# Kernel tuning notes

Hardware: AMD Instinct MI355X
Metric: run time of the kernel (lower is better)

Reference implementation:

```python
import jax, jax.numpy as jnp
import numpy as np

B, H, S, D = 2, 12, 4096, 768
BS = 64              # block size
HD = D // H          # head dim = 64
NB = S // BS         # 64 blocks
MC = 3               # max graph connections per block
PEN = -10000.0
RSQRT_D = 1.0 / np.sqrt(HD).astype(np.float32)


def setup_inputs() -> dict:
    key = jax.random.key(0)
    ks = jax.random.split(key, 6)
    hidden_states = jax.random.normal(ks[0], (B, S, D), jnp.float32)
    Wq = jax.random.normal(ks[1], (D, D), jnp.float32) * 0.02
    Wk = jax.random.normal(ks[2], (D, D), jnp.float32) * 0.02
    Wv = jax.random.normal(ks[3], (D, D), jnp.float32) * 0.02
    Wo = jax.random.normal(ks[4], (D, D), jnp.float32) * 0.02
    graph_attn = jax.random.randint(ks[5], (B, H, NB, MC), 0, NB, jnp.int32)
    return dict(
        hidden_states=hidden_states, Wq=Wq, Wk=Wk, Wv=Wv, Wo=Wo,
        band_mask=jnp.ones((B, 1, NB - 4, BS, 3 * BS), jnp.float32),
        from_mask=jnp.ones((B, 1, S, 1), jnp.float32),
        to_mask=jnp.ones((B, 1, 1, S), jnp.float32),
        from_blocked_mask=jnp.ones((B, NB, BS), jnp.float32),
        to_blocked_mask=jnp.ones((B, NB, BS), jnp.float32),
        graph_attn=graph_attn,
    )


def reference(hidden_states, Wq, Wk, Wv, Wo, band_mask, from_mask, to_mask,
              from_blocked_mask, to_blocked_mask, graph_attn):
    def proj(W):  # [B,S,D] -> [B,H,S,HD]
        return (hidden_states @ W.T).reshape(B, S, H, HD).transpose(0, 2, 1, 3)

    q, k, v = proj(Wq), proj(Wk), proj(Wv)
    bq = q.reshape(B, H, NB, BS, HD)
    bk = k.reshape(B, H, NB, BS, HD)
    bv = v.reshape(B, H, NB, BS, HD)

    # gather graph-selected key/value blocks: [B,H,NB,MC*BS,HD]
    gather = jax.vmap(jax.vmap(lambda blocks, idx: blocks[idx]))
    gk = gather(bk, graph_attn).reshape(B, H, NB, MC * BS, HD)
    gv = gather(bv, graph_attn).reshape(B, H, NB, MC * BS, HD)

    # graph mask from blocked masks: [B,H,NB,BS,MC*BS]
    gm = jax.vmap(lambda tm, ga: tm[ga])(to_blocked_mask, graph_attn)  # [B,H,NB,MC,BS]
    gm = gm.reshape(B, H, NB, MC * BS)
    graph_mask = jnp.einsum('blq,bhlk->bhlqk', from_blocked_mask, gm)

    # ---- first block: global attention over all keys ----
    fp = jnp.einsum('bhqd,bhkd->bhqk', bq[:, :, 0], k) * RSQRT_D + (1.0 - to_mask) * PEN
    first_ctx = jnp.einsum('bhqk,bhkd->bhqd', jax.nn.softmax(fp, -1), v)[:, :, None]

    # ---- second block: blocks 0,1,2,last + graph-gathered ----
    sk = jnp.concatenate([bk[:, :, 0], bk[:, :, 1], bk[:, :, 2], bk[:, :, -1], gk[:, :, 1]], axis=2)
    sv = jnp.concatenate([bv[:, :, 0], bv[:, :, 1], bv[:, :, 2], bv[:, :, -1], gv[:, :, 1]], axis=2)
    sp = jnp.einsum('bhqd,bhkd->bhqk', bq[:, :, 1], sk) * RSQRT_D
    seq_pad = jnp.concatenate([to_mask[:, :, :, :3 * BS], to_mask[:, :, :, -BS:],
                               jnp.ones((B, 1, 1, MC * BS), to_mask.dtype)], axis=3)
    rand_pad = jnp.concatenate([jnp.ones((B, H, BS, 4 * BS), graph_mask.dtype),
                                graph_mask[:, :, 1]], axis=3)
    sp = sp + (1.0 - jnp.minimum(seq_pad, rand_pad)) * PEN
    second_ctx = jnp.einsum('bhqk,bhkd->bhqd', jax.nn.softmax(sp, -1), sv)[:, :, None]

    # ---- middle blocks: sliding window (3 blocks) + first + last + graph ----
    ek = jnp.concatenate([bk[:, :, 1:-3], bk[:, :, 2:-2], bk[:, :, 3:-1]], axis=3)  # [B,H,NB-4,3BS,HD]
    ev = jnp.concatenate([bv[:, :, 1:-3], bv[:, :, 2:-2], bv[:, :, 3:-1]], axis=3)
    qm = bq[:, :, 2:-2]
    inner = jnp.einsum('bhlqd,bhlkd->bhlqk', qm, ek) * RSQRT_D + (1.0 - band_mask) * PEN
    randp = jnp.einsum('bhlqd,bhlkd->bhlqk', qm, gk[:, :, 2:-2]) * RSQRT_D + (1.0 - graph_mask[:, :, 2:-2]) * PEN
    firstp = jnp.einsum('bhlqd,bhkd->bhlqk', qm, bk[:, :, 0]) * RSQRT_D + (1.0 - to_mask[:, :, :, None, :BS]) * PEN
    lastp = jnp.einsum('bhlqd,bhkd->bhlqk', qm, bk[:, :, -1]) * RSQRT_D + (1.0 - to_mask[:, :, :, None, -BS:]) * PEN
    band = jnp.concatenate([firstp, inner, randp, lastp], axis=-1)
    attn = jax.nn.softmax(band, -1)
    mid_ctx = (jnp.einsum('bhlqk,bhlkd->bhlqd', attn[..., BS:4 * BS], ev)
               + jnp.einsum('bhlqk,bhlkd->bhlqd', attn[..., 4 * BS:4 * BS + MC * BS], gv[:, :, 2:-2])
               + jnp.einsum('bhlqk,bhkd->bhlqd', attn[..., :BS], bv[:, :, 0])
               + jnp.einsum('bhlqk,bhkd->bhlqd', attn[..., -BS:], bv[:, :, -1]))

    # ---- second-to-last block ----
    slk = jnp.concatenate([bk[:, :, 0], bk[:, :, -3], bk[:, :, -2], bk[:, :, -1], gk[:, :, -2]], axis=2)
    slv = jnp.concatenate([bv[:, :, 0], bv[:, :, -3], bv[:, :, -2], bv[:, :, -1], gv[:, :, -2]], axis=2)
    slp = jnp.einsum('bhqd,bhkd->bhqk', bq[:, :, -2], slk) * RSQRT_D
    sl_seq = jnp.concatenate([to_mask[:, :, :, :BS], to_mask[:, :, :, -3 * BS:],
                              jnp.ones((B, 1, 1, MC * BS), to_mask.dtype)], axis=3)
    sl_rand = jnp.concatenate([jnp.ones((B, H, BS, 4 * BS), graph_mask.dtype),
                               graph_mask[:, :, -2]], axis=3)
    slp = slp + (1.0 - jnp.minimum(sl_seq, sl_rand)) * PEN
    sl_ctx = jnp.einsum('bhqk,bhkd->bhqd', jax.nn.softmax(slp, -1), slv)[:, :, None]

    # ---- last block: global attention over all keys ----
    lp = jnp.einsum('bhqd,bhkd->bhqk', bq[:, :, -1], k) * RSQRT_D + (1.0 - to_mask) * PEN
    last_ctx = jnp.einsum('bhqk,bhkd->bhqd', jax.nn.softmax(lp, -1), v)[:, :, None]

    ctx = jnp.concatenate([first_ctx, second_ctx, mid_ctx, sl_ctx, last_ctx], axis=2)
    ctx = ctx.reshape(B, H, S, HD) * from_mask            # [B,H,S,HD]
    ctx = ctx.transpose(0, 2, 1, 3).reshape(B, S, D)      # [B,S,D]
    return ctx @ Wo.T                                     # output projection (no bias)
```

## Files before the change

kernel.cpp:

```cpp
#include <hip/hip_runtime.h>
#include <hip/hip_bf16.h>

#define BB 2
#define HH 12
#define SS 4096
#define DD 768
#define HD 64
#define NBK 64
#define MC 3

typedef __attribute__((ext_vector_type(8))) short short8_t;
typedef __attribute__((ext_vector_type(4))) float float4_t;

__device__ __forceinline__ unsigned short f2bf(float f) {
  union { float f; unsigned u; } c;
  c.f = f;
  unsigned u = c.u + 0x7FFFu + ((c.u >> 16) & 1u);
  return (unsigned short)(u >> 16);
}

__device__ __forceinline__ void gload16(const unsigned short* gp,
                                        unsigned short* lp) {
  __builtin_amdgcn_global_load_lds(
      (const __attribute__((address_space(1))) unsigned int*)gp,
      (__attribute__((address_space(3))) unsigned int*)lp, 16, 0, 0);
}

#define LDK 72

__global__ __launch_bounds__(256) void cvt_all(
    const float* __restrict__ hs, const float* __restrict__ Wq,
    const float* __restrict__ Wk, const float* __restrict__ Wv,
    const float* __restrict__ Wo, unsigned short* __restrict__ hsb,
    unsigned short* __restrict__ wqkvb, unsigned short* __restrict__ wob) {
  long i4 = (long)blockIdx.x * 256 + threadIdx.x;
  const float* src;
  unsigned short* dst;
  if (i4 < 1572864) {
    src = hs + i4 * 4;
    dst = hsb + i4 * 4;
  } else {
    long r = i4 - 1572864;
    int w = (int)(r / 147456);
    long e = r % 147456;
    src = (w == 0 ? Wq : w == 1 ? Wk : w == 2 ? Wv : Wo) + e * 4;
    dst = (w < 3) ? (wqkvb + (long)w * 589824 + e * 4) : (wob + e * 4);
  }
  float4_t v = *(const float4_t*)src;
  uint2 p;
  p.x = (unsigned)f2bf(v[0]) | ((unsigned)f2bf(v[1]) << 16);
  p.y = (unsigned)f2bf(v[2]) | ((unsigned)f2bf(v[3]) << 16);
  *(uint2*)dst = p;
}

#define STAGE_T(buf_, A_, B_, m0_, n0_, kt_)                                  \
  {                                                                           \
    int rr_ = lane >> 3;                                                      \
    int cg_ = (lane & 7) ^ rr_;                                               \
    _Pragma("unroll") for (int u = 0; u < 4; u++) {                           \
      int g_ = w * 4 + u;                                                     \
      gload16(A_ + (size_t)(m0_ + g_ * 8 + rr_) * DD + kt_ + cg_ * 8,         \
              &As[buf_][g_ * 512]);                                           \
    }                                                                         \
    _Pragma("unroll") for (int u = 0; u < 2; u++) {                           \
      int g_ = w * 2 + u;                                                     \
      gload16(B_ + (size_t)(n0_ + g_ * 8 + rr_) * DD + kt_ + cg_ * 8,         \
              &Bs[buf_][g_ * 512]);                                           \
    }                                                                         \
  }

#define LOAD_FRAGS2(buf_, kk_)                                                \
  int cb = qd + ((kk_) >> 3);                                                 \
  short8_t af[2], bfr[4];                                                     \
  _Pragma("unroll") for (int i = 0; i < 2; i++) {                             \
    int r_ = wm + i * 16 + fr;                                                \
    af[i] = *(const short8_t*)&As[buf_][r_ * 64 + (cb ^ (fr & 7)) * 8];       \
  }                                                                           \
  _Pragma("unroll") for (int j = 0; j < 4; j++) {                             \
    int r_ = j * 16 + fr;                                                     \
    bfr[j] = *(const short8_t*)&Bs[buf_][r_ * 64 + (cb ^ (fr & 7)) * 8];      \
  }

__global__ __launch_bounds__(256) void gemm_qkv_b(
    const unsigned short* __restrict__ A, const unsigned short* __restrict__ W,
    unsigned short* __restrict__ qb, unsigned short* __restrict__ kb,
    unsigned short* __restrict__ vtb) {
  __shared__ unsigned short As[2][128 * 64];
  __shared__ unsigned short Bs[2][64 * 64];
  int tid = threadIdx.x;
  int m0 = blockIdx.x * 128;
  int n0 = blockIdx.y * 64;
  int lane = tid & 63;
  int w = tid >> 6;
  int wm = w * 32;
  int fr = lane & 15;
  int qd = lane >> 4;
  int ysel = n0 / 768;

  float4_t acc[8];
#pragma unroll
  for (int i = 0; i < 8; i++)
#pragma unroll
    for (int r = 0; r < 4; r++) acc[i][r] = 0.f;

  STAGE_T(0, A, W, m0, n0, 0)
  int p = 0;

  if (ysel < 2) {
    for (int kt = 0; kt < DD; kt += 64) {
      __syncthreads();
      if (kt + 64 < DD) STAGE_T(p ^ 1, A, W, m0, n0, kt + 64)
#pragma unroll
      for (int kk = 0; kk < 64; kk += 32) {
        LOAD_FRAGS2(p, kk)
#pragma unroll
        for (int i = 0; i < 2; i++)
#pragma unroll
          for (int j = 0; j < 4; j++)
            acc[j * 2 + i] = __builtin_amdgcn_mfma_f32_16x16x32_bf16(
                bfr[j], af[i], acc[j * 2 + i], 0, 0, 0);
      }
      p ^= 1;
    }
    int cn = lane & 15;
    int quad = lane >> 4;
    float scale = (ysel == 0) ? 0.125f : 1.0f;
    unsigned short* dst = (ysel == 0) ? qb : kb;
    int nb0 = n0 - ysel * 768;
#pragma unroll
    for (int j = 0; j < 4; j++)
#pragma unroll
      for (int i = 0; i < 2; i++) {
        int m = m0 + wm + i * 16 + cn;
        int nn = nb0 + j * 16 + quad * 4;
        int b = m >> 12, s = m & 4095;
        int h = nn >> 6, d0 = nn & 63;
        uint2 pk;
        pk.x = (unsigned)f2bf(acc[j * 2 + i][0] * scale) |
               ((unsigned)f2bf(acc[j * 2 + i][1] * scale) << 16);
        pk.y = (unsigned)f2bf(acc[j * 2 + i][2] * scale) |
               ((unsigned)f2bf(acc[j * 2 + i][3] * scale) << 16);
        *(uint2*)&dst[(((size_t)b * HH + h) * SS + s) * HD + d0] = pk;
      }
  } else {
    for (int kt = 0; kt < DD; kt += 64) {
      __syncthreads();
      if (kt + 64 < DD) STAGE_T(p ^ 1, A, W, m0, n0, kt + 64)
#pragma unroll
      for (int kk = 0; kk < 64; kk += 32) {
        LOAD_FRAGS2(p, kk)
#pragma unroll
        for (int i = 0; i < 2; i++)
#pragma unroll
          for (int j = 0; j < 4; j++)
            acc[i * 4 + j] = __builtin_amdgcn_mfma_f32_16x16x32_bf16(
                af[i], bfr[j], acc[i * 4 + j], 0, 0, 0);
      }
      p ^= 1;
    }
    int cn = lane & 15;
    int quad = lane >> 4;
    int nb0 = n0 - 1536;
#pragma unroll
    for (int i = 0; i < 2; i++)
#pragma unroll
      for (int j = 0; j < 4; j++) {
        int m = m0 + wm + i * 16 + quad * 4;
        int nn = nb0 + j * 16 + cn;
        int b = m >> 12, s0 = m & 4095;
        int h = nn >> 6, d = nn & 63;
        uint2 pk;
        pk.x = (unsigned)f2bf(acc[i * 4 + j][0]) |
               ((unsigned)f2bf(acc[i * 4 + j][1]) << 16);
        pk.y = (unsigned)f2bf(acc[i * 4 + j][2]) |
               ((unsigned)f2bf(acc[i * 4 + j][3]) << 16);
        *(uint2*)&vtb[(((size_t)b * HH + h) * HD + d) * SS + s0] = pk;
      }
  }
}

__global__ __launch_bounds__(256) void gemm_out_b(
    const unsigned short* __restrict__ A, const unsigned short* __restrict__ W,
    float* __restrict__ dst) {
  __shared__ unsigned short As[2][128 * 64];
  __shared__ unsigned short Bs[2][64 * 64];
  int tid = threadIdx.x;
  int m0 = blockIdx.x * 128;
  int n0 = blockIdx.y * 64;
  int lane = tid & 63;
  int w = tid >> 6;
  int wm = w * 32;
  int fr = lane & 15;
  int qd = lane >> 4;

  float4_t acc[8];
#pragma unroll
  for (int i = 0; i < 8; i++)
#pragma unroll
    for (int r = 0; r < 4; r++) acc[i][r] = 0.f;

  STAGE_T(0, A, W, m0, n0, 0)
  int p = 0;
  for (int kt = 0; kt < DD; kt += 64) {
    __syncthreads();
    if (kt + 64 < DD) STAGE_T(p ^ 1, A, W, m0, n0, kt + 64)
#pragma unroll
    for (int kk = 0; kk < 64; kk += 32) {
      LOAD_FRAGS2(p, kk)
#pragma unroll
      for (int i = 0; i < 2; i++)
#pragma unroll
        for (int j = 0; j < 4; j++)
          acc[i * 4 + j] = __builtin_amdgcn_mfma_f32_16x16x32_bf16(
              af[i], bfr[j], acc[i * 4 + j], 0, 0, 0);
    }
    p ^= 1;
  }

  int cn = lane & 15;
  int rb = (lane >> 4) * 4;
#pragma unroll
  for (int i = 0; i < 2; i++)
#pragma unroll
    for (int j = 0; j < 4; j++)
#pragma unroll
      for (int r = 0; r < 4; r++) {
        int m = m0 + wm + i * 16 + rb + r;
        int n = n0 + j * 16 + cn;
        dst[(size_t)m * DD + n] = acc[i * 4 + j][r];
      }
}

__global__ __launch_bounds__(256) void attn2(
    const unsigned short* __restrict__ q, const unsigned short* __restrict__ k,
    const unsigned short* __restrict__ vt, const int* __restrict__ graph,
    unsigned short* __restrict__ ctxb, float* __restrict__ part) {
  __shared__ unsigned short Ks[2][64 * LDK];
  __shared__ unsigned short Vs[2][64 * LDK];
  __shared__ unsigned short Ps[4][16 * LDK];

  int tid = threadIdx.x;
  int id = blockIdx.x;
  int b, h, l, nkb, heavy, chunk = 0, hid = 0;
  int list[8];
  if (id < 384) {
    heavy = 1;
    hid = id >> 3;
    chunk = id & 7;
    b = hid / 24;
    int r = hid % 24;
    h = r >> 1;
    l = (r & 1) ? (NBK - 1) : 0;
    nkb = 8;
#pragma unroll
    for (int i = 0; i < 8; i++) list[i] = chunk * 8 + i;
  } else {
    heavy = 0;
    int j = id - 384;
    b = j / 744;
    int r = j % 744;
    h = r / 62;
    l = 1 + r % 62;
    const int* g = graph + (((size_t)b * HH + h) * NBK + l) * MC;
    int n = 0;
    if (l == 1) {
      list[0] = 0; list[1] = 1; list[2] = 2; list[3] = NBK - 1; n = 4;
    } else if (l == NBK - 2) {
      list[0] = 0; list[1] = NBK - 3; list[2] = NBK - 2; list[3] = NBK - 1; n = 4;
    } else {
      list[0] = 0; list[1] = l - 1; list[2] = l; list[3] = l + 1;
      list[4] = NBK - 1; n = 5;
    }
    for (int m = 0; m < MC; m++) list[n++] = g[m];
    nkb = n;
  }
  size_t base = ((size_t)b * HH + h) * SS * HD;

  int lane = tid & 63;
  int w = tid >> 6;
  int lr = lane & 15;
  int quad = lane >> 4;

  short8_t qa[2];
  {
    const unsigned short* qp =
        q + base + (size_t)(l * 64 + w * 16 + lr) * HD + quad * 8;
    qa[0] = *(const short8_t*)qp;
    qa[1] = *(const short8_t*)(qp + 32);
  }

  float4_t Ot[4];
  float ls[4];
#pragma unroll
  for (int t = 0; t < 4; t++)
#pragma unroll
    for (int r = 0; r < 4; r++) Ot[t][r] = 0.f;
#pragma unroll
  for (int r = 0; r < 4; r++) ls[r] = 0.f;

  int srow = tid >> 3;
  int scol = (tid & 7) * 8;

  uint4 kr0, kr1, vr0, vr1;
  {
    int kb = list[0];
    const unsigned short* kp = k + base + (size_t)(kb * 64 + srow) * HD + scol;
    const unsigned short* vp = vt + base + (size_t)srow * SS + kb * 64 + scol;
    kr0 = *(const uint4*)kp;
    kr1 = *(const uint4*)(kp + 32 * HD);
    vr0 = *(const uint4*)vp;
    vr1 = *(const uint4*)(vp + 32 * SS);
  }
  *(uint4*)&Ks[0][srow * LDK + scol] = kr0;
  *(uint4*)&Ks[0][(srow + 32) * LDK + scol] = kr1;
  *(uint4*)&Vs[0][srow * LDK + scol] = vr0;
  *(uint4*)&Vs[0][(srow + 32) * LDK + scol] = vr1;
  int p = 0;

  for (int t = 0; t < nkb; t++) {
    __syncthreads();

    if (t + 1 < nkb) {
      int kb = list[t + 1];
      const unsigned short* kp = k + base + (size_t)(kb * 64 + srow) * HD + scol;
      const unsigned short* vp = vt + base + (size_t)srow * SS + kb * 64 + scol;
      kr0 = *(const uint4*)kp;
      kr1 = *(const uint4*)(kp + 32 * HD);
      vr0 = *(const uint4*)vp;
      vr1 = *(const uint4*)(vp + 32 * SS);
    }

    float4_t st[4];
#pragma unroll
    for (int tt = 0; tt < 4; tt++) {
#pragma unroll
      for (int r = 0; r < 4; r++) st[tt][r] = 0.f;
      short8_t kb0 = *(const short8_t*)&Ks[p][(tt * 16 + lr) * LDK + quad * 8];
      short8_t kb1 =
          *(const short8_t*)&Ks[p][(tt * 16 + lr) * LDK + quad * 8 + 32];
      st[tt] = __builtin_amdgcn_mfma_f32_16x16x32_bf16(qa[0], kb0, st[tt], 0, 0, 0);
      st[tt] = __builtin_amdgcn_mfma_f32_16x16x32_bf16(qa[1], kb1, st[tt], 0, 0, 0);
    }

#pragma unroll
    for (int tt = 0; tt < 4; tt++)
#pragma unroll
      for (int r = 0; r < 4; r++) {
        float pv = __expf(st[tt][r]);
        st[tt][r] = pv;
        ls[r] += pv;
        Ps[w][(quad * 4 + r) * LDK + tt * 16 + lr] = f2bf(pv);
      }

#pragma unroll
    for (int s = 0; s < 2; s++) {
      short8_t pa = *(const short8_t*)&Ps[w][lr * LDK + s * 32 + quad * 8];
#pragma unroll
      for (int tt = 0; tt < 4; tt++) {
        short8_t vb =
            *(const short8_t*)&Vs[p][(tt * 16 + lr) * LDK + s * 32 + quad * 8];
        Ot[tt] = __builtin_amdgcn_mfma_f32_16x16x32_bf16(pa, vb, Ot[tt], 0, 0, 0);
      }
    }

    if (t + 1 < nkb) {
      *(uint4*)&Ks[p ^ 1][srow * LDK + scol] = kr0;
      *(uint4*)&Ks[p ^ 1][(srow + 32) * LDK + scol] = kr1;
      *(uint4*)&Vs[p ^ 1][srow * LDK + scol] = vr0;
      *(uint4*)&Vs[p ^ 1][(srow + 32) * LDK + scol] = vr1;
    }
    p ^= 1;
  }

#pragma unroll
  for (int r = 0; r < 4; r++)
#pragma unroll
    for (int off = 1; off < 16; off <<= 1) ls[r] += __shfl_xor(ls[r], off);

  if (!heavy) {
#pragma unroll
    for (int r = 0; r < 4; r++) {
      float inv = 1.f / ls[r];
      size_t row = (size_t)b * SS + (size_t)l * 64 + w * 16 + quad * 4 + r;
#pragma unroll
      for (int tt = 0; tt < 4; tt++)
        ctxb[row * DD + h * HD + tt * 16 + lr] = f2bf(Ot[tt][r] * inv);
    }
  } else {
    float* pb = part + ((size_t)hid * 8 + chunk) * 4160;
#pragma unroll
    for (int r = 0; r < 4; r++) {
      int rowi = w * 16 + quad * 4 + r;
#pragma unroll
      for (int tt = 0; tt < 4; tt++)
        pb[rowi * 64 + tt * 16 + lr] = Ot[tt][r];
      if (lr == 0) pb[4096 + rowi] = ls[r];
    }
  }
}

__global__ __launch_bounds__(256) void reduce_heavy(
    const float* __restrict__ part, unsigned short* __restrict__ ctxb) {
  __shared__ float lrow[64];
  int hid = blockIdx.x;
  int tid = threadIdx.x;
  int b = hid / 24;
  int r = hid % 24;
  int h = r >> 1;
  int l = (r & 1) ? (NBK - 1) : 0;
  const float* pb = part + (size_t)hid * 8 * 4160;
  if (tid < 64) {
    float s = 0.f;
#pragma unroll
    for (int c = 0; c < 8; c++) s += pb[c * 4160 + 4096 + tid];
    lrow[tid] = s;
  }
  __syncthreads();
#pragma unroll
  for (int e = tid; e < 4096; e += 256) {
    float o = 0.f;
#pragma unroll
    for (int c = 0; c < 8; c++) o += pb[c * 4160 + e];
    int rowi = e >> 6, col = e & 63;
    size_t row = (size_t)b * SS + (size_t)l * 64 + rowi;
    ctxb[row * DD + h * HD + col] = f2bf(o / lrow[rowi]);
  }
}

extern "C" void kernel_launch(void* const* d_in, const int* in_sizes, int n_in,
                              void* d_out, int out_size, void* d_ws,
                              size_t ws_size, hipStream_t stream) {
  const float* hs = (const float*)d_in[0];
  const float* Wq = (const float*)d_in[1];
  const float* Wk = (const float*)d_in[2];
  const float* Wv = (const float*)d_in[3];
  const float* Wo = (const float*)d_in[4];
  const int* graph = (const int*)d_in[10];

  const size_t NHS = (size_t)BB * SS * DD;
  unsigned short* hsb = (unsigned short*)d_ws;
  unsigned short* wqkvb = hsb + NHS;
  unsigned short* wob = wqkvb + 3 * 768 * 768;
  unsigned short* qb = wob + 768 * 768;
  unsigned short* kb = qb + NHS;
  unsigned short* vtb = kb + NHS;
  unsigned short* ctxb = vtb + NHS;
  float* part = (float*)(ctxb + NHS);

  cvt_all<<<8448, 256, 0, stream>>>(hs, Wq, Wk, Wv, Wo, hsb, wqkvb, wob);
  gemm_qkv_b<<<dim3(64, 36, 1), 256, 0, stream>>>(hsb, wqkvb, qb, kb, vtb);
  attn2<<<1872, 256, 0, stream>>>(qb, kb, vtb, graph, ctxb, part);
  reduce_heavy<<<48, 256, 0, stream>>>(part, ctxb);
  gemm_out_b<<<dim3(64, 12, 1), 256, 0, stream>>>(ctxb, wob, (float*)d_out);
}
```

Baseline: 209.5 us.

## Fuse all stages into one persistent cooperative kernel with grid syncs

Replaces the five separate launches (convert, QKV GEMM, attention, heavy-row reduce, output GEMM) with a single persistent cooperative kernel. Blocks loop over virtual tiles per stage and use grid.sync between stages. The goal is to remove kernel launch gaps and inter-kernel drain. In exchange, the grid is capped by occupancy, the grid-wide barriers add cost, and the unified 48KB shared buffer may lower occupancy for the attention stage. The old multi-kernel path is kept as a fallback if the cooperative launch fails.

```diff
diff --git a/kernel.cpp b/kernel.cpp
--- a/kernel.cpp
+++ b/kernel.cpp
@@ -1,5 +1,8 @@
 #include <hip/hip_runtime.h>
 #include <hip/hip_bf16.h>
+#include <hip/hip_cooperative_groups.h>
+
+namespace cg = cooperative_groups;
 
 #define BB 2
 #define HH 12
@@ -8,6 +11,7 @@
 #define HD 64
 #define NBK 64
 #define MC 3
+#define LDK 72
 
 typedef __attribute__((ext_vector_type(8))) short short8_t;
 typedef __attribute__((ext_vector_type(4))) float float4_t;
@@ -26,7 +30,433 @@
       (__attribute__((address_space(3))) unsigned int*)lp, 16, 0, 0);
 }
 
-#define LDK 72
+
+__device__ __forceinline__ void stage_ab(unsigned short* AsB, unsigned short* BsB,
+                                         const unsigned short* A,
+                                         const unsigned short* B, int m0,
+                                         int n0, int kt, int lane, int w) {
+  int rr = lane >> 3;
+  int cgx = (lane & 7) ^ rr;
+#pragma unroll
+  for (int u = 0; u < 4; u++) {
+    int g = w * 4 + u;
+    gload16(A + (size_t)(m0 + g * 8 + rr) * DD + kt + cgx * 8, AsB + g * 512);
+  }
+#pragma unroll
+  for (int u = 0; u < 2; u++) {
+    int g = w * 2 + u;
+    gload16(B + (size_t)(n0 + g * 8 + rr) * DD + kt + cgx * 8, BsB + g * 512);
+  }
+}
+
+template <int SWAP>
+__device__ __forceinline__ void gemm_core(const unsigned short* A,
+                                          const unsigned short* B, int m0,
+                                          int n0, unsigned short* smem,
+                                          int tid, float4_t acc[8]) {
+  unsigned short* As = smem;
+  unsigned short* Bs = smem + 16384;
+  int lane = tid & 63;
+  int w = tid >> 6;
+  int wm = w * 32;
+  int fr = lane & 15;
+  int qd = lane >> 4;
+#pragma unroll
+  for (int i = 0; i < 8; i++)
+#pragma unroll
+    for (int r = 0; r < 4; r++) acc[i][r] = 0.f;
+  __syncthreads();
+  stage_ab(As, Bs, A, B, m0, n0, 0, lane, w);
+  int p = 0;
+  for (int kt = 0; kt < DD; kt += 64) {
+    __syncthreads();
+    if (kt + 64 < DD)
+      stage_ab(As + (p ^ 1) * 8192, Bs + (p ^ 1) * 4096, A, B, m0, n0, kt + 64,
+               lane, w);
+#pragma unroll
+    for (int kk = 0; kk < 64; kk += 32) {
+      int cb = qd + (kk >> 3);
+      short8_t af[2], bfr[4];
+#pragma unroll
+      for (int i = 0; i < 2; i++) {
+        int r_ = wm + i * 16 + fr;
+        af[i] =
+            *(const short8_t*)&As[p * 8192 + r_ * 64 + (cb ^ (fr & 7)) * 8];
+      }
+#pragma unroll
+      for (int j = 0; j < 4; j++) {
+        int r_ = j * 16 + fr;
+        bfr[j] =
+            *(const short8_t*)&Bs[p * 4096 + r_ * 64 + (cb ^ (fr & 7)) * 8];
+      }
+#pragma unroll
+      for (int i = 0; i < 2; i++)
+#pragma unroll
+        for (int j = 0; j < 4; j++) {
+          if (SWAP)
+            acc[j * 2 + i] = __builtin_amdgcn_mfma_f32_16x16x32_bf16(
+                bfr[j], af[i], acc[j * 2 + i], 0, 0, 0);
+          else
+            acc[i * 4 + j] = __builtin_amdgcn_mfma_f32_16x16x32_bf16(
+                af[i], bfr[j], acc[i * 4 + j], 0, 0, 0);
+        }
+    }
+    p ^= 1;
+  }
+}
+
+__device__ __forceinline__ void qkv_tile(int vb, const unsigned short* hsb,
+                                         const unsigned short* wqkvb,
+                                         unsigned short* qb,
+                                         unsigned short* kb,
+                                         unsigned short* vtb,
+                                         unsigned short* smem, int tid) {
+  int m0 = (vb & 63) * 128;
+  int n0 = (vb >> 6) * 64;
+  int ysel = n0 / 768;
+  int lane = tid & 63;
+  int w = tid >> 6;
+  int wm = w * 32;
+  float4_t acc[8];
+  if (ysel < 2) {
+    gemm_core<1>(hsb, wqkvb, m0, n0, smem, tid, acc);
+    int cn = lane & 15;
+    int quad = lane >> 4;
+    float scale = (ysel == 0) ? 0.125f : 1.0f;
+    unsigned short* dst = (ysel == 0) ? qb : kb;
+    int nb0 = n0 - ysel * 768;
+#pragma unroll
+    for (int j = 0; j < 4; j++)
+#pragma unroll
+      for (int i = 0; i < 2; i++) {
+        int m = m0 + wm + i * 16 + cn;
+        int nn = nb0 + j * 16 + quad * 4;
+        int b = m >> 12, s = m & 4095;
+        int h = nn >> 6, d0 = nn & 63;
+        uint2 pk;
+        pk.x = (unsigned)f2bf(acc[j * 2 + i][0] * scale) |
+               ((unsigned)f2bf(acc[j * 2 + i][1] * scale) << 16);
+        pk.y = (unsigned)f2bf(acc[j * 2 + i][2] * scale) |
+               ((unsigned)f2bf(acc[j * 2 + i][3] * scale) << 16);
+        *(uint2*)&dst[(((size_t)b * HH + h) * SS + s) * HD + d0] = pk;
+      }
+  } else {
+    gemm_core<0>(hsb, wqkvb, m0, n0, smem, tid, acc);
+    int cn = lane & 15;
+    int quad = lane >> 4;
+    int nb0 = n0 - 1536;
+#pragma unroll
+    for (int i = 0; i < 2; i++)
+#pragma unroll
+      for (int j = 0; j < 4; j++) {
+        int m = m0 + wm + i * 16 + quad * 4;
+        int nn = nb0 + j * 16 + cn;
+        int b = m >> 12, s0 = m & 4095;
+        int h = nn >> 6, d = nn & 63;
+        uint2 pk;
+        pk.x = (unsigned)f2bf(acc[i * 4 + j][0]) |
+               ((unsigned)f2bf(acc[i * 4 + j][1]) << 16);
+        pk.y = (unsigned)f2bf(acc[i * 4 + j][2]) |
+               ((unsigned)f2bf(acc[i * 4 + j][3]) << 16);
+        *(uint2*)&vtb[(((size_t)b * HH + h) * HD + d) * SS + s0] = pk;
+      }
+  }
+}
+
+__device__ __forceinline__ void out_tile(int vb, const unsigned short* ctxb,
+                                         const unsigned short* wob,
+                                         float* dst, unsigned short* smem,
+                                         int tid) {
+  int m0 = (vb & 63) * 128;
+  int n0 = (vb >> 6) * 64;
+  float4_t acc[8];
+  gemm_core<0>(ctxb, wob, m0, n0, smem, tid, acc);
+  int lane = tid & 63;
+  int w = tid >> 6;
+  int wm = w * 32;
+  int cn = lane & 15;
+  int rb = (lane >> 4) * 4;
+#pragma unroll
+  for (int i = 0; i < 2; i++)
+#pragma unroll
+    for (int j = 0; j < 4; j++)
+#pragma unroll
+      for (int r = 0; r < 4; r++) {
+        int m = m0 + wm + i * 16 + rb + r;
+        int n = n0 + j * 16 + cn;
+        dst[(size_t)m * DD + n] = acc[i * 4 + j][r];
+      }
+}
+
+__device__ __forceinline__ void attn_one(int id, const unsigned short* q,
+                                         const unsigned short* k,
+                                         const unsigned short* vt,
+                                         const int* graph,
+                                         unsigned short* ctxb, float* part,
+                                         unsigned short* smem, int tid) {
+  unsigned short* Ks = smem;
+  unsigned short* Vs = smem + 2 * 64 * LDK;
+  unsigned short* Ps = smem + 4 * 64 * LDK;
+  int b, h, l, nkb, heavy, chunk = 0, hid = 0;
+  int list[8];
+  if (id < 384) {
+    heavy = 1;
+    hid = id >> 3;
+    chunk = id & 7;
+    b = hid / 24;
+    int r = hid % 24;
+    h = r >> 1;
+    l = (r & 1) ? (NBK - 1) : 0;
+    nkb = 8;
+#pragma unroll
+    for (int i = 0; i < 8; i++) list[i] = chunk * 8 + i;
+  } else {
+    heavy = 0;
+    int j = id - 384;
+    b = j / 744;
+    int r = j % 744;
+    h = r / 62;
+    l = 1 + r % 62;
+    const int* g = graph + (((size_t)b * HH + h) * NBK + l) * MC;
+    int n = 0;
+    if (l == 1) {
+      list[0] = 0; list[1] = 1; list[2] = 2; list[3] = NBK - 1; n = 4;
+    } else if (l == NBK - 2) {
+      list[0] = 0; list[1] = NBK - 3; list[2] = NBK - 2; list[3] = NBK - 1;
+      n = 4;
+    } else {
+      list[0] = 0; list[1] = l - 1; list[2] = l; list[3] = l + 1;
+      list[4] = NBK - 1; n = 5;
+    }
+    for (int m = 0; m < MC; m++) list[n++] = g[m];
+    nkb = n;
+  }
+  size_t base = ((size_t)b * HH + h) * SS * HD;
+
+  int lane = tid & 63;
+  int w = tid >> 6;
+  int lr = lane & 15;
+  int quad = lane >> 4;
+
+  short8_t qa[2];
+  {
+    const unsigned short* qp =
+        q + base + (size_t)(l * 64 + w * 16 + lr) * HD + quad * 8;
+    qa[0] = *(const short8_t*)qp;
+    qa[1] = *(const short8_t*)(qp + 32);
+  }
+
+  float4_t Ot[4];
+  float ls[4];
+#pragma unroll
+  for (int t = 0; t < 4; t++)
+#pragma unroll
+    for (int r = 0; r < 4; r++) Ot[t][r] = 0.f;
+#pragma unroll
+  for (int r = 0; r < 4; r++) ls[r] = 0.f;
+
+  int srow = tid >> 3;
+  int scol = (tid & 7) * 8;
+
+  uint4 kr0, kr1, vr0, vr1;
+  {
+    int kb = list[0];
+    const unsigned short* kp = k + base + (size_t)(kb * 64 + srow) * HD + scol;
+    const unsigned short* vp = vt + base + (size_t)srow * SS + kb * 64 + scol;
+    kr0 = *(const uint4*)kp;
+    kr1 = *(const uint4*)(kp + 32 * HD);
+    vr0 = *(const uint4*)vp;
+    vr1 = *(const uint4*)(vp + 32 * SS);
+  }
+  __syncthreads();
+  *(uint4*)&Ks[srow * LDK + scol] = kr0;
+  *(uint4*)&Ks[(srow + 32) * LDK + scol] = kr1;
+  *(uint4*)&Vs[srow * LDK + scol] = vr0;
+  *(uint4*)&Vs[(srow + 32) * LDK + scol] = vr1;
+  int p = 0;
+
+  for (int t = 0; t < nkb; t++) {
+    __syncthreads();
+
+    if (t + 1 < nkb) {
+      int kb = list[t + 1];
+      const unsigned short* kp =
+          k + base + (size_t)(kb * 64 + srow) * HD + scol;
+      const unsigned short* vp =
+          vt + base + (size_t)srow * SS + kb * 64 + scol;
+      kr0 = *(const uint4*)kp;
+      kr1 = *(const uint4*)(kp + 32 * HD);
+      vr0 = *(const uint4*)vp;
+      vr1 = *(const uint4*)(vp + 32 * SS);
+    }
+
+    float4_t st[4];
+#pragma unroll
+    for (int tt = 0; tt < 4; tt++) {
+#pragma unroll
+      for (int r = 0; r < 4; r++) st[tt][r] = 0.f;
+      short8_t kb0 =
+          *(const short8_t*)&Ks[p * 4608 + (tt * 16 + lr) * LDK + quad * 8];
+      short8_t kb1 = *(const short8_t*)&Ks[p * 4608 + (tt * 16 + lr) * LDK +
+                                           quad * 8 + 32];
+      st[tt] =
+          __builtin_amdgcn_mfma_f32_16x16x32_bf16(qa[0], kb0, st[tt], 0, 0, 0);
+      st[tt] =
+          __builtin_amdgcn_mfma_f32_16x16x32_bf16(qa[1], kb1, st[tt], 0, 0, 0);
+    }
+
+#pragma unroll
+    for (int tt = 0; tt < 4; tt++)
+#pragma unroll
+      for (int r = 0; r < 4; r++) {
+        float pv = __expf(st[tt][r]);
+        st[tt][r] = pv;
+        ls[r] += pv;
+        Ps[w * 1152 + (quad * 4 + r) * LDK + tt * 16 + lr] = f2bf(pv);
+      }
+
+#pragma unroll
+    for (int s = 0; s < 2; s++) {
+      short8_t pa =
+          *(const short8_t*)&Ps[w * 1152 + lr * LDK + s * 32 + quad * 8];
+#pragma unroll
+      for (int tt = 0; tt < 4; tt++) {
+        short8_t vb = *(const short8_t*)&Vs[p * 4608 + (tt * 16 + lr) * LDK +
+                                            s * 32 + quad * 8];
+        Ot[tt] =
+            __builtin_amdgcn_mfma_f32_16x16x32_bf16(pa, vb, Ot[tt], 0, 0, 0);
+      }
+    }
+
+    if (t + 1 < nkb) {
+      int pn = p ^ 1;
+      *(uint4*)&Ks[pn * 4608 + srow * LDK + scol] = kr0;
+      *(uint4*)&Ks[pn * 4608 + (srow + 32) * LDK + scol] = kr1;
+      *(uint4*)&Vs[pn * 4608 + srow * LDK + scol] = vr0;
+      *(uint4*)&Vs[pn * 4608 + (srow + 32) * LDK + scol] = vr1;
+    }
+    p ^= 1;
+  }
+
+#pragma unroll
+  for (int r = 0; r < 4; r++)
+#pragma unroll
+    for (int off = 1; off < 16; off <<= 1) ls[r] += __shfl_xor(ls[r], off);
+
+  if (!heavy) {
+#pragma unroll
+    for (int r = 0; r < 4; r++) {
+      float inv = 1.f / ls[r];
+      size_t row = (size_t)b * SS + (size_t)l * 64 + w * 16 + quad * 4 + r;
+#pragma unroll
+      for (int tt = 0; tt < 4; tt++)
+        ctxb[row * DD + h * HD + tt * 16 + lr] = f2bf(Ot[tt][r] * inv);
+    }
+  } else {
+    float* pb = part + ((size_t)hid * 8 + chunk) * 4160;
+#pragma unroll
+    for (int r = 0; r < 4; r++) {
+      int rowi = w * 16 + quad * 4 + r;
+#pragma unroll
+      for (int tt = 0; tt < 4; tt++)
+        pb[rowi * 64 + tt * 16 + lr] = Ot[tt][r];
+      if (lr == 0) pb[4096 + rowi] = ls[r];
+    }
+  }
+}
+
+__device__ __forceinline__ void reduce_one(int hid, const float* part,
+                                           unsigned short* ctxb,
+                                           unsigned short* smem, int tid) {
+  float* lrow = (float*)smem;
+  int b = hid / 24;
+  int r = hid % 24;
+  int h = r >> 1;
+  int l = (r & 1) ? (NBK - 1) : 0;
+  const float* pb = part + (size_t)hid * 8 * 4160;
+  __syncthreads();
+  if (tid < 64) {
+    float s = 0.f;
+#pragma unroll
+    for (int c = 0; c < 8; c++) s += pb[c * 4160 + 4096 + tid];
+    lrow[tid] = s;
+  }
+  __syncthreads();
+  for (int e = tid; e < 4096; e += 256) {
+    float o = 0.f;
+#pragma unroll
+    for (int c = 0; c < 8; c++) o += pb[c * 4160 + e];
+    int rowi = e >> 6, col = e & 63;
+    size_t row = (size_t)b * SS + (size_t)l * 64 + rowi;
+    ctxb[row * DD + h * HD + col] = f2bf(o / lrow[rowi]);
+  }
+  __syncthreads();
+}
+
+__global__ __launch_bounds__(256) void fused_all(
+    const float* __restrict__ hs, const float* __restrict__ Wq,
+    const float* __restrict__ Wk, const float* __restrict__ Wv,
+    const float* __restrict__ Wo, const int* __restrict__ graph,
+    float* __restrict__ dst, unsigned short* __restrict__ wsu) {
+  __shared__ __align__(16) unsigned short smem[24576];
+  int tid = threadIdx.x;
+  int wg = blockIdx.x;
+  int gsz = gridDim.x;
+  const size_t NHS = (size_t)BB * SS * DD;
+  unsigned short* hsb = wsu;
+  unsigned short* wqkvb = hsb + NHS;
+  unsigned short* wob = wqkvb + 3 * 768 * 768;
+  unsigned short* qb = wob + 768 * 768;
+  unsigned short* kb = qb + NHS;
+  unsigned short* vtb = kb + NHS;
+  unsigned short* ctxb = vtb + NHS;
+  float* part = (float*)(ctxb + NHS);
+  cg::grid_group grid = cg::this_grid();
+
+  for (long i4 = (long)wg * 256 + tid; i4 < 2162688; i4 += (long)gsz * 256) {
+    const float* src;
+    unsigned short* dp;
+    if (i4 < 1572864) {
+      src = hs + i4 * 4;
+      dp = hsb + i4 * 4;
+    } else {
+      long r = i4 - 1572864;
+      int wsel = (int)(r / 147456);
+      long e = r % 147456;
+      src = (wsel == 0 ? Wq : wsel == 1 ? Wk : wsel == 2 ? Wv : Wo) + e * 4;
+      dp = (wsel < 3) ? (wqkvb + (long)wsel * 589824 + e * 4) : (wob + e * 4);
+    }
+    float4_t v = *(const float4_t*)src;
+    uint2 pk;
+    pk.x = (unsigned)f2bf(v[0]) | ((unsigned)f2bf(v[1]) << 16);
+    pk.y = (unsigned)f2bf(v[2]) | ((unsigned)f2bf(v[3]) << 16);
+    *(uint2*)dp = pk;
+  }
+  __threadfence();
+  grid.sync();
+  __threadfence();
+
+  for (int vb = wg; vb < 2304; vb += gsz)
+    qkv_tile(vb, hsb, wqkvb, qb, kb, vtb, smem, tid);
+  __threadfence();
+  grid.sync();
+  __threadfence();
+
+  for (int vb = wg; vb < 1872; vb += gsz)
+    attn_one(vb, qb, kb, vtb, graph, ctxb, part, smem, tid);
+  __threadfence();
+  grid.sync();
+  __threadfence();
+
+  for (int vb = wg; vb < 48; vb += gsz) reduce_one(vb, part, ctxb, smem, tid);
+  __threadfence();
+  grid.sync();
+  __threadfence();
+
+  for (int vb = wg; vb < 768; vb += gsz)
+    out_tile(vb, ctxb, wob, dst, smem, tid);
+}
+
 
 __global__ __launch_bounds__(256) void cvt_all(
     const float* __restrict__ hs, const float* __restrict__ Wq,
@@ -53,378 +483,35 @@
   *(uint2*)dst = p;
 }
 
-#define STAGE_T(buf_, A_, B_, m0_, n0_, kt_)                                  \
-  {                                                                           \
-    int rr_ = lane >> 3;                                                      \
-    int cg_ = (lane & 7) ^ rr_;                                               \
-    _Pragma("unroll") for (int u = 0; u < 4; u++) {                           \
-      int g_ = w * 4 + u;                                                     \
-      gload16(A_ + (size_t)(m0_ + g_ * 8 + rr_) * DD + kt_ + cg_ * 8,         \
-              &As[buf_][g_ * 512]);                                           \
-    }                                                                         \
-    _Pragma("unroll") for (int u = 0; u < 2; u++) {                           \
-      int g_ = w * 2 + u;                                                     \
-      gload16(B_ + (size_t)(n0_ + g_ * 8 + rr_) * DD + kt_ + cg_ * 8,         \
-              &Bs[buf_][g_ * 512]);                                           \
-    }                                                                         \
-  }
-
-#define LOAD_FRAGS2(buf_, kk_)                                                \
-  int cb = qd + ((kk_) >> 3);                                                 \
-  short8_t af[2], bfr[4];                                                     \
-  _Pragma("unroll") for (int i = 0; i < 2; i++) {                             \
-    int r_ = wm + i * 16 + fr;                                                \
-    af[i] = *(const short8_t*)&As[buf_][r_ * 64 + (cb ^ (fr & 7)) * 8];       \
-  }                                                                           \
-  _Pragma("unroll") for (int j = 0; j < 4; j++) {                             \
-    int r_ = j * 16 + fr;                                                     \
-    bfr[j] = *(const short8_t*)&Bs[buf_][r_ * 64 + (cb ^ (fr & 7)) * 8];      \
-  }
-
 __global__ __launch_bounds__(256) void gemm_qkv_b(
     const unsigned short* __restrict__ A, const unsigned short* __restrict__ W,
     unsigned short* __restrict__ qb, unsigned short* __restrict__ kb,
     unsigned short* __restrict__ vtb) {
-  __shared__ unsigned short As[2][128 * 64];
-  __shared__ unsigned short Bs[2][64 * 64];
-  int tid = threadIdx.x;
-  int m0 = blockIdx.x * 128;
-  int n0 = blockIdx.y * 64;
-  int lane = tid & 63;
-  int w = tid >> 6;
-  int wm = w * 32;
-  int fr = lane & 15;
-  int qd = lane >> 4;
-  int ysel = n0 / 768;
-
-  float4_t acc[8];
-#pragma unroll
-  for (int i = 0; i < 8; i++)
-#pragma unroll
-    for (int r = 0; r < 4; r++) acc[i][r] = 0.f;
-
-  STAGE_T(0, A, W, m0, n0, 0)
-  int p = 0;
-
-  if (ysel < 2) {
-    for (int kt = 0; kt < DD; kt += 64) {
-      __syncthreads();
-      if (kt + 64 < DD) STAGE_T(p ^ 1, A, W, m0, n0, kt + 64)
-#pragma unroll
-      for (int kk = 0; kk < 64; kk += 32) {
-        LOAD_FRAGS2(p, kk)
-#pragma unroll
-        for (int i = 0; i < 2; i++)
-#pragma unroll
-          for (int j = 0; j < 4; j++)
-            acc[j * 2 + i] = __builtin_amdgcn_mfma_f32_16x16x32_bf16(
-                bfr[j], af[i], acc[j * 2 + i], 0, 0, 0);
-      }
-      p ^= 1;
-    }
-    int cn = lane & 15;
-    int quad = lane >> 4;
-    float scale = (ysel == 0) ? 0.125f : 1.0f;
-    unsigned short* dst = (ysel == 0) ? qb : kb;
-    int nb0 = n0 - ysel * 768;
-#pragma unroll
-    for (int j = 0; j < 4; j++)
-#pragma unroll
-      for (int i = 0; i < 2; i++) {
-        int m = m0 + wm + i * 16 + cn;
-        int nn = nb0 + j * 16 + quad * 4;
-        int b = m >> 12, s = m & 4095;
-        int h = nn >> 6, d0 = nn & 63;
-        uint2 pk;
-        pk.x = (unsigned)f2bf(acc[j * 2 + i][0] * scale) |
-               ((unsigned)f2bf(acc[j * 2 + i][1] * scale) << 16);
-        pk.y = (unsigned)f2bf(acc[j * 2 + i][2] * scale) |
-               ((unsigned)f2bf(acc[j * 2 + i][3] * scale) << 16);
-        *(uint2*)&dst[(((size_t)b * HH + h) * SS + s) * HD + d0] = pk;
-      }
-  } else {
-    for (int kt = 0; kt < DD; kt += 64) {
-      __syncthreads();
-      if (kt + 64 < DD) STAGE_T(p ^ 1, A, W, m0, n0, kt + 64)
-#pragma unroll
-      for (int kk = 0; kk < 64; kk += 32) {
-        LOAD_FRAGS2(p, kk)
-#pragma unroll
-        for (int i = 0; i < 2; i++)
-#pragma unroll
-          for (int j = 0; j < 4; j++)
-            acc[i * 4 + j] = __builtin_amdgcn_mfma_f32_16x16x32_bf16(
-                af[i], bfr[j], acc[i * 4 + j], 0, 0, 0);
-      }
-      p ^= 1;
-    }
-    int cn = lane & 15;
-    int quad = lane >> 4;
-    int nb0 = n0 - 1536;
-#pragma unroll
-    for (int i = 0; i < 2; i++)
-#pragma unroll
-      for (int j = 0; j < 4; j++) {
-        int m = m0 + wm + i * 16 + quad * 4;
-        int nn = nb0 + j * 16 + cn;
-        int b = m >> 12, s0 = m & 4095;
-        int h = nn >> 6, d = nn & 63;
-        uint2 pk;
-        pk.x = (unsigned)f2bf(acc[i * 4 + j][0]) |
-               ((unsigned)f2bf(acc[i * 4 + j][1]) << 16);
-        pk.y = (unsigned)f2bf(acc[i * 4 + j][2]) |
-               ((unsigned)f2bf(acc[i * 4 + j][3]) << 16);
-        *(uint2*)&vtb[(((size_t)b * HH + h) * HD + d) * SS + s0] = pk;
-      }
-  }
+  __shared__ __align__(16) unsigned short smem[24576];
+  int vb = blockIdx.x + blockIdx.y * 64;
+  qkv_tile(vb, A, W, qb, kb, vtb, smem, threadIdx.x);
 }
 
 __global__ __launch_bounds__(256) void gemm_out_b(
     const unsigned short* __restrict__ A, const unsigned short* __restrict__ W,
     float* __restrict__ dst) {
-  __shared__ unsigned short As[2][128 * 64];
-  __shared__ unsigned short Bs[2][64 * 64];
-  int tid = threadIdx.x;
-  int m0 = blockIdx.x * 128;
-  int n0 = blockIdx.y * 64;
-  int lane = tid & 63;
-  int w = tid >> 6;
-  int wm = w * 32;
-  int fr = lane & 15;
-  int qd = lane >> 4;
-
-  float4_t acc[8];
-#pragma unroll
-  for (int i = 0; i < 8; i++)
-#pragma unroll
-    for (int r = 0; r < 4; r++) acc[i][r] = 0.f;
-
-  STAGE_T(0, A, W, m0, n0, 0)
-  int p = 0;
-  for (int kt = 0; kt < DD; kt += 64) {
-    __syncthreads();
-    if (kt + 64 < DD) STAGE_T(p ^ 1, A, W, m0, n0, kt + 64)
-#pragma unroll
-    for (int kk = 0; kk < 64; kk += 32) {
-      LOAD_FRAGS2(p, kk)
-#pragma unroll
-      for (int i = 0; i < 2; i++)
-#pragma unroll
-        for (int j = 0; j < 4; j++)
-          acc[i * 4 + j] = __builtin_amdgcn_mfma_f32_16x16x32_bf16(
-              af[i], bfr[j], acc[i * 4 + j], 0, 0, 0);
-    }
-    p ^= 1;
-  }
-
-  int cn = lane & 15;
-  int rb = (lane >> 4) * 4;
-#pragma unroll
-  for (int i = 0; i < 2; i++)
-#pragma unroll
-    for (int j = 0; j < 4; j++)
-#pragma unroll
-      for (int r = 0; r < 4; r++) {
-        int m = m0 + wm + i * 16 + rb + r;
-        int n = n0 + j * 16 + cn;
-        dst[(size_t)m * DD + n] = acc[i * 4 + j][r];
-      }
+  __shared__ __align__(16) unsigned short smem[24576];
+  int vb = blockIdx.x + blockIdx.y * 64;
+  out_tile(vb, A, W, dst, smem, threadIdx.x);
 }
 
 __global__ __launch_bounds__(256) void attn2(
     const unsigned short* __restrict__ q, const unsigned short* __restrict__ k,
     const unsigned short* __restrict__ vt, const int* __restrict__ graph,
     unsigned short* __restrict__ ctxb, float* __restrict__ part) {
-  __shared__ unsigned short Ks[2][64 * LDK];
-  __shared__ unsigned short Vs[2][64 * LDK];
-  __shared__ unsigned short Ps[4][16 * LDK];
-
-  int tid = threadIdx.x;
-  int id = blockIdx.x;
-  int b, h, l, nkb, heavy, chunk = 0, hid = 0;
-  int list[8];
-  if (id < 384) {
-    heavy = 1;
-    hid = id >> 3;
-    chunk = id & 7;
-    b = hid / 24;
-    int r = hid % 24;
-    h = r >> 1;
-    l = (r & 1) ? (NBK - 1) : 0;
-    nkb = 8;
-#pragma unroll
-    for (int i = 0; i < 8; i++) list[i] = chunk * 8 + i;
-  } else {
-    heavy = 0;
-    int j = id - 384;
-    b = j / 744;
-    int r = j % 744;
-    h = r / 62;
-    l = 1 + r % 62;
-    const int* g = graph + (((size_t)b * HH + h) * NBK + l) * MC;
-    int n = 0;
-    if (l == 1) {
-      list[0] = 0; list[1] = 1; list[2] = 2; list[3] = NBK - 1; n = 4;
-    } else if (l == NBK - 2) {
-      list[0] = 0; list[1] = NBK - 3; list[2] = NBK - 2; list[3] = NBK - 1; n = 4;
-    } else {
-      list[0] = 0; list[1] = l - 1; list[2] = l; list[3] = l + 1;
-      list[4] = NBK - 1; n = 5;
-    }
-    for (int m = 0; m < MC; m++) list[n++] = g[m];
-    nkb = n;
-  }
-  size_t base = ((size_t)b * HH + h) * SS * HD;
-
-  int lane = tid & 63;
-  int w = tid >> 6;
-  int lr = lane & 15;
-  int quad = lane >> 4;
-
-  short8_t qa[2];
-  {
-    const unsigned short* qp =
-        q + base + (size_t)(l * 64 + w * 16 + lr) * HD + quad * 8;
-    qa[0] = *(const short8_t*)qp;
-    qa[1] = *(const short8_t*)(qp + 32);
-  }
-
-  float4_t Ot[4];
-  float ls[4];
-#pragma unroll
-  for (int t = 0; t < 4; t++)
-#pragma unroll
-    for (int r = 0; r < 4; r++) Ot[t][r] = 0.f;
-#pragma unroll
-  for (int r = 0; r < 4; r++) ls[r] = 0.f;
-
-  int srow = tid >> 3;
-  int scol = (tid & 7) * 8;
-
-  uint4 kr0, kr1, vr0, vr1;
-  {
-    int kb = list[0];
-    const unsigned short* kp = k + base + (size_t)(kb * 64 + srow) * HD + scol;
-    const unsigned short* vp = vt + base + (size_t)srow * SS + kb * 64 + scol;
-    kr0 = *(const uint4*)kp;
-    kr1 = *(const uint4*)(kp + 32 * HD);
-    vr0 = *(const uint4*)vp;
-    vr1 = *(const uint4*)(vp + 32 * SS);
-  }
-  *(uint4*)&Ks[0][srow * LDK + scol] = kr0;
-  *(uint4*)&Ks[0][(srow + 32) * LDK + scol] = kr1;
-  *(uint4*)&Vs[0][srow * LDK + scol] = vr0;
-  *(uint4*)&Vs[0][(srow + 32) * LDK + scol] = vr1;
-  int p = 0;
-
-  for (int t = 0; t < nkb; t++) {
-    __syncthreads();
-
-    if (t + 1 < nkb) {
-      int kb = list[t + 1];
-      const unsigned short* kp = k + base + (size_t)(kb * 64 + srow) * HD + scol;
-      const unsigned short* vp = vt + base + (size_t)srow * SS + kb * 64 + scol;
-      kr0 = *(const uint4*)kp;
-      kr1 = *(const uint4*)(kp + 32 * HD);
-      vr0 = *(const uint4*)vp;
-      vr1 = *(const uint4*)(vp + 32 * SS);
-    }
-
-    float4_t st[4];
-#pragma unroll
-    for (int tt = 0; tt < 4; tt++) {
-#pragma unroll
-      for (int r = 0; r < 4; r++) st[tt][r] = 0.f;
-      short8_t kb0 = *(const short8_t*)&Ks[p][(tt * 16 + lr) * LDK + quad * 8];
-      short8_t kb1 =
-          *(const short8_t*)&Ks[p][(tt * 16 + lr) * LDK + quad * 8 + 32];
-      st[tt] = __builtin_amdgcn_mfma_f32_16x16x32_bf16(qa[0], kb0, st[tt], 0, 0, 0);
-      st[tt] = __builtin_amdgcn_mfma_f32_16x16x32_bf16(qa[1], kb1, st[tt], 0, 0, 0);
-    }
-
-#pragma unroll
-    for (int tt = 0; tt < 4; tt++)
-#pragma unroll
-      for (int r = 0; r < 4; r++) {
-        float pv = __expf(st[tt][r]);
-        st[tt][r] = pv;
-        ls[r] += pv;
-        Ps[w][(quad * 4 + r) * LDK + tt * 16 + lr] = f2bf(pv);
-      }
-
-#pragma unroll
-    for (int s = 0; s < 2; s++) {
-      short8_t pa = *(const short8_t*)&Ps[w][lr * LDK + s * 32 + quad * 8];
-#pragma unroll
-      for (int tt = 0; tt < 4; tt++) {
-        short8_t vb =
-            *(const short8_t*)&Vs[p][(tt * 16 + lr) * LDK + s * 32 + quad * 8];
-        Ot[tt] = __builtin_amdgcn_mfma_f32_16x16x32_bf16(pa, vb, Ot[tt], 0, 0, 0);
-      }
-    }
-
-    if (t + 1 < nkb) {
-      *(uint4*)&Ks[p ^ 1][srow * LDK + scol] = kr0;
-      *(uint4*)&Ks[p ^ 1][(srow + 32) * LDK + scol] = kr1;
-      *(uint4*)&Vs[p ^ 1][srow * LDK + scol] = vr0;
-      *(uint4*)&Vs[p ^ 1][(srow + 32) * LDK + scol] = vr1;
-    }
-    p ^= 1;
-  }
-
-#pragma unroll
-  for (int r = 0; r < 4; r++)
-#pragma unroll
-    for (int off = 1; off < 16; off <<= 1) ls[r] += __shfl_xor(ls[r], off);
-
-  if (!heavy) {
-#pragma unroll
-    for (int r = 0; r < 4; r++) {
-      float inv = 1.f / ls[r];
-      size_t row = (size_t)b * SS + (size_t)l * 64 + w * 16 + quad * 4 + r;
-#pragma unroll
-      for (int tt = 0; tt < 4; tt++)
-        ctxb[row * DD + h * HD + tt * 16 + lr] = f2bf(Ot[tt][r] * inv);
-    }
-  } else {
-    float* pb = part + ((size_t)hid * 8 + chunk) * 4160;
-#pragma unroll
-    for (int r = 0; r < 4; r++) {
-      int rowi = w * 16 + quad * 4 + r;
-#pragma unroll
-      for (int tt = 0; tt < 4; tt++)
-        pb[rowi * 64 + tt * 16 + lr] = Ot[tt][r];
-      if (lr == 0) pb[4096 + rowi] = ls[r];
-    }
-  }
+  __shared__ __align__(16) unsigned short smem[24576];
+  attn_one(blockIdx.x, q, k, vt, graph, ctxb, part, smem, threadIdx.x);
 }
 
 __global__ __launch_bounds__(256) void reduce_heavy(
     const float* __restrict__ part, unsigned short* __restrict__ ctxb) {
-  __shared__ float lrow[64];
-  int hid = blockIdx.x;
-  int tid = threadIdx.x;
-  int b = hid / 24;
-  int r = hid % 24;
-  int h = r >> 1;
-  int l = (r & 1) ? (NBK - 1) : 0;
-  const float* pb = part + (size_t)hid * 8 * 4160;
-  if (tid < 64) {
-    float s = 0.f;
-#pragma unroll
-    for (int c = 0; c < 8; c++) s += pb[c * 4160 + 4096 + tid];
-    lrow[tid] = s;
-  }
-  __syncthreads();
-#pragma unroll
-  for (int e = tid; e < 4096; e += 256) {
-    float o = 0.f;
-#pragma unroll
-    for (int c = 0; c < 8; c++) o += pb[c * 4160 + e];
-    int rowi = e >> 6, col = e & 63;
-    size_t row = (size_t)b * SS + (size_t)l * 64 + rowi;
-    ctxb[row * DD + h * HD + col] = f2bf(o / lrow[rowi]);
-  }
+  __shared__ __align__(16) unsigned short smem[24576];
+  reduce_one(blockIdx.x, part, ctxb, smem, threadIdx.x);
 }
 
 extern "C" void kernel_launch(void* const* d_in, const int* in_sizes, int n_in,
@@ -436,9 +523,32 @@
   const float* Wv = (const float*)d_in[3];
   const float* Wo = (const float*)d_in[4];
   const int* graph = (const int*)d_in[10];
+  unsigned short* wsu = (unsigned short*)d_ws;
+  float* dst = (float*)d_out;
+
+  int nb = 0;
+  hipError_t oe =
+      hipOccupancyMaxActiveBlocksPerMultiprocessor(&nb, fused_all, 256, 0);
+  if (oe == hipSuccess && nb >= 1) {
+    int gridn = nb * 256;
+    if (gridn > 2304) gridn = 2304;
+    void* args[8];
+    args[0] = (void*)&hs;
+    args[1] = (void*)&Wq;
+    args[2] = (void*)&Wk;
+    args[3] = (void*)&Wv;
+    args[4] = (void*)&Wo;
+    args[5] = (void*)&graph;
+    args[6] = (void*)&dst;
+    args[7] = (void*)&wsu;
+    hipError_t le = hipLaunchCooperativeKernel(
+        (const void*)fused_all, dim3(gridn, 1, 1), dim3(256, 1, 1), args, 0,
+        stream);
+    if (le == hipSuccess) return;
+  }
 
   const size_t NHS = (size_t)BB * SS * DD;
-  unsigned short* hsb = (unsigned short*)d_ws;
+  unsigned short* hsb = wsu;
   unsigned short* wqkvb = hsb + NHS;
   unsigned short* wob = wqkvb + 3 * 768 * 768;
   unsigned short* qb = wob + 768 * 768;
@@ -451,5 +561,5 @@
   gemm_qkv_b<<<dim3(64, 36, 1), 256, 0, stream>>>(hsb, wqkvb, qb, kb, vtb);
   attn2<<<1872, 256, 0, stream>>>(qb, kb, vtb, graph, ctxb, part);
   reduce_heavy<<<48, 256, 0, stream>>>(part, ctxb);
-  gemm_out_b<<<dim3(64, 12, 1), 256, 0, stream>>>(ctxb, wob, (float*)d_out);
-}
+  gemm_out_b<<<dim3(64, 12, 1), 256, 0, stream>>>(ctxb, wob, dst);
+}
```

Measured after the change: 199.5 us. -4.8%, faster.
